# Optimization experiments

Measured on AMD Instinct MI355X. Metric: run time of the kernel, lower is better.

The kernel has to match this reference:

```python
import jax, jax.numpy as jnp
import numpy as np

COMMITMENT_COST = 0.25
NUM_EMBEDDINGS = 1024
EMBEDDING_DIM = 256


def setup_inputs() -> dict:
    key = jax.random.key(0)
    k1, k2 = jax.random.split(key)
    inputs = jax.random.normal(k1, (64, 256, 32, 32), dtype=jnp.float32)
    emb_w = jax.random.normal(k2, (NUM_EMBEDDINGS, EMBEDDING_DIM), dtype=jnp.float32)
    return {"inputs": inputs, "emb_w": emb_w}


def reference(inputs, emb_w):
    # NCHW -> NHWC, flatten to [N, D]
    x = jnp.transpose(inputs, (0, 2, 3, 1))  # [B, H, W, D]
    B, H, W, D = x.shape
    flat = x.reshape(-1, D)  # [N, D]

    distances = (
        jnp.sum(flat * flat, axis=1, keepdims=True)
        + jnp.sum(emb_w * emb_w, axis=1)
        - 2.0 * flat @ emb_w.T
    )
    idx = jnp.argmin(distances, axis=1)  # [N]

    # one-hot @ W is just a gather of codebook rows
    quantized = emb_w[idx].reshape(B, H, W, D)

    # avg_probs = mean of one-hot encodings = normalized codeword counts
    counts = jnp.zeros((NUM_EMBEDDINGS,), dtype=jnp.float32).at[idx].add(1.0)
    avg_probs = counts / flat.shape[0]
    perplexity = jnp.exp(-jnp.sum(avg_probs * jnp.log(avg_probs + 1e-10)))

    e_latent_loss = jnp.mean((jax.lax.stop_gradient(quantized) - x) ** 2)
    loss = COMMITMENT_COST * e_latent_loss

    # straight-through estimator
    quantized_st = x + jax.lax.stop_gradient(quantized - x)
    quantized_out = jnp.transpose(quantized_st, (0, 3, 1, 2))  # back to NCHW

    return loss, quantized_out, perplexity, idx.reshape(B, H, W)
```

## Files before the change

### kernel.cpp

```cpp
#include <hip/hip_runtime.h>
#include <hip/hip_bf16.h>
#include <math.h>

typedef _Float16 f16;
typedef __attribute__((ext_vector_type(8))) _Float16 f16x8;
typedef __attribute__((ext_vector_type(16))) float f32x16;

#define DIMS 256
#define NCODE 1024
#define NPTS 65536

#define OUT_Q_OFF 1
#define OUT_PERP_OFF 16777217
#define OUT_IDX_OFF 16777218

#define EHI_F32_OFF 4
#define ELO_F32_OFF (4 + 131072)
#define TILE_BYTES 16384

#define XSTRIDE 132

__device__ __forceinline__ void gload_lds16(const void* g, void* l) {
    __builtin_amdgcn_global_load_lds(
        (const __attribute__((address_space(1))) unsigned int*)g,
        (__attribute__((address_space(3))) unsigned int*)l, 16, 0, 0);
}

__global__ __launch_bounds__(256) void k_eprep(const float* __restrict__ ew,
                                               char* __restrict__ ehi,
                                               char* __restrict__ elo,
                                               float* __restrict__ enorm) {
    int w = threadIdx.x >> 6;
    int l = threadIdx.x & 63;
    int row = blockIdx.x * 4 + w;
    float4 v = *reinterpret_cast<const float4*>(ew + (size_t)row * DIMS + l * 4);
    float vv[4] = {v.x, v.y, v.z, v.w};
    __align__(8) f16 hh[4];
    __align__(8) f16 ll[4];
    float s = 0.0f;
    #pragma unroll
    for (int e = 0; e < 4; ++e) {
        f16 h = (f16)vv[e];
        hh[e] = h;
        ll[e] = (f16)(vv[e] - (float)h);
        s += vv[e] * vv[e];
    }
    size_t off = (size_t)(row >> 5) * TILE_BYTES + (size_t)(row & 31) * 512
               + (size_t)((((l >> 1) ^ (row & 7)) << 4) + ((l & 1) << 3));
    *reinterpret_cast<float2*>(ehi + off) = *reinterpret_cast<float2*>(hh);
    *reinterpret_cast<float2*>(elo + off) = *reinterpret_cast<float2*>(ll);
    #pragma unroll
    for (int off2 = 32; off2 > 0; off2 >>= 1) s += __shfl_down(s, off2);
    if (l == 0) enorm[row] = s;
}

__global__ __launch_bounds__(256, 2) void k_argmin_mfma(const float* __restrict__ x,
                                                        const char* __restrict__ ehi,
                                                        const char* __restrict__ elo,
                                                        const float* __restrict__ enorm,
                                                        int* __restrict__ out_idx) {
    __shared__ __align__(16) char smem[2 * 2 * TILE_BYTES];
    __shared__ float enorm_lds[NCODE];
    float* Xs = (float*)smem;

    const int t = threadIdx.x;
    const int wave = t >> 6;
    const int lane = t & 63;
    const int lrow = lane & 31;
    const int lhalf = lane >> 5;

    const int blk = blockIdx.x;
    const int b = blk >> 3;
    const int hw0 = (blk & 7) << 7;
    const float* xb = x + (size_t)b * (DIMS * 1024) + hw0;

    #pragma unroll
    for (int i = 0; i < 4; ++i) enorm_lds[t + 256 * i] = enorm[t + 256 * i];

    f16x8 ahi[16], alo[16];
    #pragma unroll
    for (int dc = 0; dc < 4; ++dc) {
        __syncthreads();
        #pragma unroll
        for (int i = 0; i < 8; ++i) {
            int d = (t >> 5) + 8 * i;
            int p4 = (t & 31) * 4;
            float4 v = *reinterpret_cast<const float4*>(xb + (size_t)(dc * 64 + d) * 1024 + p4);
            *reinterpret_cast<float4*>(&Xs[d * XSTRIDE + p4]) = v;
        }
        __syncthreads();
        int p = wave * 32 + lrow;
        #pragma unroll
        for (int kcl = 0; kcl < 4; ++kcl) {
            f16x8 h, l;
            #pragma unroll
            for (int e = 0; e < 8; ++e) {
                float xv = Xs[(kcl * 16 + lhalf * 8 + e) * XSTRIDE + p];
                f16 hi = (f16)xv;
                h[e] = hi;
                l[e] = (f16)(xv - (float)hi);
            }
            ahi[dc * 4 + kcl] = h;
            alo[dc * 4 + kcl] = l;
        }
    }
    __syncthreads();

    const char* gplane = (wave >> 1) ? elo : ehi;
    const int pl_off = (wave >> 1) * TILE_BYTES;
    const int woff = (wave & 1) * 8192;

    #pragma unroll
    for (int i = 0; i < 8; ++i) {
        int off = woff + i * 1024;
        gload_lds16(gplane + off + lane * 16, smem + pl_off + off);
    }
    __syncthreads();

    float bestv[16];
    int besti[16];
    #pragma unroll
    for (int r = 0; r < 16; ++r) { bestv[r] = 3.4e38f; besti[r] = 0; }

    int cur = 0;
    for (int rd = 0; rd < 32; ++rd) {
        if (rd + 1 < 32) {
            const char* gp = gplane + (size_t)(rd + 1) * TILE_BYTES;
            char* lp = smem + (cur ^ 1) * (2 * TILE_BYTES) + pl_off;
            #pragma unroll
            for (int i = 0; i < 8; ++i) {
                int off = woff + i * 1024;
                gload_lds16(gp + off + lane * 16, lp + off);
            }
        }

        const char* EHb = smem + cur * (2 * TILE_BYTES);
        const char* ELb = EHb + TILE_BYTES;
        f32x16 acc;
        #pragma unroll
        for (int r = 0; r < 16; ++r) acc[r] = 0.0f;

        #pragma unroll
        for (int kc = 0; kc < 16; ++kc) {
            int g = kc * 2 + lhalf;
            int ra = lrow * 512 + ((g ^ (lrow & 7)) << 4);
            f16x8 bh = *reinterpret_cast<const f16x8*>(EHb + ra);
            f16x8 bl = *reinterpret_cast<const f16x8*>(ELb + ra);
            acc = __builtin_amdgcn_mfma_f32_32x32x16_f16(ahi[kc], bh, acc, 0, 0, 0);
            acc = __builtin_amdgcn_mfma_f32_32x32x16_f16(ahi[kc], bl, acc, 0, 0, 0);
            acc = __builtin_amdgcn_mfma_f32_32x32x16_f16(alo[kc], bh, acc, 0, 0, 0);
        }

        const int code0 = rd * 32;
        float en = enorm_lds[code0 + lrow];
        int cw = code0 + lrow;
        #pragma unroll
        for (int r = 0; r < 16; ++r) {
            float s = fmaf(-2.0f, acc[r], en);
            if (s < bestv[r]) { bestv[r] = s; besti[r] = cw; }
        }

        __syncthreads();
        cur ^= 1;
    }

    #pragma unroll
    for (int off = 1; off <= 16; off <<= 1) {
        #pragma unroll
        for (int r = 0; r < 16; ++r) {
            float ov = __shfl_xor(bestv[r], off);
            int oi = __shfl_xor(besti[r], off);
            if (ov < bestv[r] || (ov == bestv[r] && oi < besti[r])) {
                bestv[r] = ov;
                besti[r] = oi;
            }
        }
    }
    if (lrow == 0) {
        #pragma unroll
        for (int r = 0; r < 16; ++r) {
            int row = (r & 3) + 8 * (r >> 2) + 4 * lhalf;
            out_idx[blk * 128 + wave * 32 + row] = besti[r];
        }
    }
}

#define QSTRIDE 258
__global__ __launch_bounds__(512) void k_quant(const float* __restrict__ x,
                                               const float* __restrict__ ew,
                                               const int* __restrict__ idxv,
                                               float* __restrict__ out,
                                               float* __restrict__ loss_acc) {
    __shared__ float Eq[64 * QSTRIDE];
    __shared__ int ids[64];
    const int t = threadIdx.x;
    const int blk = blockIdx.x;
    const int b = blk >> 4;
    const int hw0 = (blk & 15) << 6;

    if (t < 64) ids[t] = idxv[(b << 10) + hw0 + t];
    __syncthreads();

    #pragma unroll
    for (int i = 0; i < 8; ++i) {
        int f = i * 512 + t;
        int row = f >> 6;
        int c4 = f & 63;
        float4 v = *reinterpret_cast<const float4*>(ew + (size_t)ids[row] * DIMS + c4 * 4);
        float2 lo2 = {v.x, v.y};
        float2 hi2 = {v.z, v.w};
        *reinterpret_cast<float2*>(&Eq[row * QSTRIDE + c4 * 4]) = lo2;
        *reinterpret_cast<float2*>(&Eq[row * QSTRIDE + c4 * 4 + 2]) = hi2;
    }
    __syncthreads();

    const int p = t & 63;
    const int c0 = t >> 6;
    float lsum = 0.0f;
    #pragma unroll
    for (int k = 0; k < 32; ++k) {
        int c = k * 8 + c0;
        unsigned g = ((unsigned)b << 18) | ((unsigned)c << 10) | (unsigned)(hw0 + p);
        float xv = x[g];
        float q = Eq[p * QSTRIDE + c];
        float d = q - xv;
        out[OUT_Q_OFF + g] = xv + d;
        lsum += d * d;
    }
    #pragma unroll
    for (int off = 32; off > 0; off >>= 1) lsum += __shfl_down(lsum, off);
    if ((t & 63) == 0) atomicAdd(&loss_acc[blk & 63], lsum);
}

__global__ __launch_bounds__(256) void k_hist(const int* __restrict__ idxv,
                                              int* __restrict__ counts,
                                              float* __restrict__ out) {
    __shared__ int h[NCODE];
    int t = threadIdx.x;
    #pragma unroll
    for (int i = 0; i < 4; ++i) h[t + 256 * i] = 0;
    __syncthreads();
    int base = blockIdx.x * 1024;
    #pragma unroll
    for (int i = 0; i < 4; ++i) {
        int n = base + t + 256 * i;
        int id = idxv[n];
        out[OUT_IDX_OFF + n] = (float)id;
        atomicAdd(&h[id], 1);
    }
    __syncthreads();
    #pragma unroll
    for (int i = 0; i < 4; ++i) {
        int v = h[t + 256 * i];
        if (v) atomicAdd(&counts[t + 256 * i], v);
    }
}

__global__ __launch_bounds__(256) void k_final(const int* __restrict__ counts,
                                               const float* __restrict__ loss_acc,
                                               float* __restrict__ out) {
    int t = threadIdx.x;
    float s = 0.0f;
    #pragma unroll
    for (int i = 0; i < 4; ++i) {
        int cnt = counts[t + 256 * i];
        float p = (float)cnt * (1.0f / 65536.0f);
        s += p * logf(p + 1e-10f);
    }
    #pragma unroll
    for (int off = 32; off > 0; off >>= 1) s += __shfl_down(s, off);
    __shared__ float wsum[4];
    if ((t & 63) == 0) wsum[t >> 6] = s;
    __syncthreads();
    if (t == 0) {
        float S = wsum[0] + wsum[1] + wsum[2] + wsum[3];
        out[OUT_PERP_OFF] = expf(-S);
        float ls = 0.0f;
        for (int i = 0; i < 64; ++i) ls += loss_acc[i];
        out[0] = 0.25f * (ls * (1.0f / 16777216.0f));
    }
}

extern "C" void kernel_launch(void* const* d_in, const int* in_sizes, int n_in,
                              void* d_out, int out_size, void* d_ws, size_t ws_size,
                              hipStream_t stream) {
    const float* x = (const float*)d_in[0];
    const float* ew = (const float*)d_in[1];
    float* out = (float*)d_out;
    float* ws = (float*)d_ws;

    float* loss_acc = ws;
    int* counts = (int*)(ws + 64);
    float* enorm = ws + 64 + 1024;
    int* idxv = (int*)(ws + 64 + 2048);

    char* ehi = (char*)(out + EHI_F32_OFF);
    char* elo = (char*)(out + ELO_F32_OFF);

    hipMemsetAsync(d_ws, 0, (64 + 1024) * sizeof(float), stream);

    k_eprep<<<256, 256, 0, stream>>>(ew, ehi, elo, enorm);
    k_argmin_mfma<<<512, 256, 0, stream>>>(x, ehi, elo, enorm, idxv);
    k_quant<<<1024, 512, 0, stream>>>(x, ew, idxv, out, loss_acc);
    k_hist<<<64, 256, 0, stream>>>(idxv, counts, out);
    k_final<<<1, 256, 0, stream>>>(counts, loss_acc, out);
}
```

Baseline: 178.4 us.

## Read low-half codebook from global directly and fuse histogram into quant kernel

The argmin kernel now stages only the high-half fp16 codebook tiles in LDS, halving the LDS footprint. The low-half tiles are read straight from global/L2 in a transposed, coalesced layout written by the prep kernel. MFMA sections get raised wave priority, and the separate histogram kernel is folded into the quant kernel with a per-block LDS histogram, removing one launch. The trade-off is extra global-load latency inside the MFMA loop in exchange for higher occupancy, plus 1024 blocks each flushing histogram atomics instead of 64.

```diff
diff --git a/kernel.cpp b/kernel.cpp
--- a/kernel.cpp
+++ b/kernel.cpp
@@ -45,10 +45,12 @@
         ll[e] = (f16)(vv[e] - (float)h);
         s += vv[e] * vv[e];
     }
-    size_t off = (size_t)(row >> 5) * TILE_BYTES + (size_t)(row & 31) * 512
-               + (size_t)((((l >> 1) ^ (row & 7)) << 4) + ((l & 1) << 3));
-    *reinterpret_cast<float2*>(ehi + off) = *reinterpret_cast<float2*>(hh);
-    *reinterpret_cast<float2*>(elo + off) = *reinterpret_cast<float2*>(ll);
+    size_t hoff = (size_t)(row >> 5) * TILE_BYTES + (size_t)(row & 31) * 512
+                + (size_t)((((l >> 1) ^ (row & 7)) << 4) + ((l & 1) << 3));
+    size_t loff = (size_t)(row >> 5) * TILE_BYTES + (size_t)(l >> 1) * 512
+                + (size_t)(((row & 31) << 4) + ((l & 1) << 3));
+    *reinterpret_cast<float2*>(ehi + hoff) = *reinterpret_cast<float2*>(hh);
+    *reinterpret_cast<float2*>(elo + loff) = *reinterpret_cast<float2*>(ll);
     #pragma unroll
     for (int off2 = 32; off2 > 0; off2 >>= 1) s += __shfl_down(s, off2);
     if (l == 0) enorm[row] = s;
@@ -59,7 +61,7 @@
                                                         const char* __restrict__ elo,
                                                         const float* __restrict__ enorm,
                                                         int* __restrict__ out_idx) {
-    __shared__ __align__(16) char smem[2 * 2 * TILE_BYTES];
+    __shared__ __align__(16) char smem[XSTRIDE * 64 * 4];
     __shared__ float enorm_lds[NCODE];
     float* Xs = (float*)smem;
 
@@ -106,14 +108,10 @@
     }
     __syncthreads();
 
-    const char* gplane = (wave >> 1) ? elo : ehi;
-    const int pl_off = (wave >> 1) * TILE_BYTES;
-    const int woff = (wave & 1) * 8192;
-
-    #pragma unroll
-    for (int i = 0; i < 8; ++i) {
-        int off = woff + i * 1024;
-        gload_lds16(gplane + off + lane * 16, smem + pl_off + off);
+    #pragma unroll
+    for (int i = 0; i < 4; ++i) {
+        int off = wave * 4096 + i * 1024;
+        gload_lds16(ehi + off + lane * 16, smem + off);
     }
     __syncthreads();
 
@@ -122,34 +120,37 @@
     #pragma unroll
     for (int r = 0; r < 16; ++r) { bestv[r] = 3.4e38f; besti[r] = 0; }
 
-    int cur = 0;
     for (int rd = 0; rd < 32; ++rd) {
+        const int cur = rd & 1;
         if (rd + 1 < 32) {
-            const char* gp = gplane + (size_t)(rd + 1) * TILE_BYTES;
-            char* lp = smem + (cur ^ 1) * (2 * TILE_BYTES) + pl_off;
+            const char* gp = ehi + (size_t)(rd + 1) * TILE_BYTES;
+            char* lp = smem + (cur ^ 1) * TILE_BYTES;
             #pragma unroll
-            for (int i = 0; i < 8; ++i) {
-                int off = woff + i * 1024;
+            for (int i = 0; i < 4; ++i) {
+                int off = wave * 4096 + i * 1024;
                 gload_lds16(gp + off + lane * 16, lp + off);
             }
         }
 
-        const char* EHb = smem + cur * (2 * TILE_BYTES);
-        const char* ELb = EHb + TILE_BYTES;
+        const char* EHb = smem + cur * TILE_BYTES;
+        const char* ELg = elo + (size_t)rd * TILE_BYTES;
         f32x16 acc;
         #pragma unroll
         for (int r = 0; r < 16; ++r) acc[r] = 0.0f;
 
+        __builtin_amdgcn_s_setprio(1);
         #pragma unroll
         for (int kc = 0; kc < 16; ++kc) {
             int g = kc * 2 + lhalf;
-            int ra = lrow * 512 + ((g ^ (lrow & 7)) << 4);
-            f16x8 bh = *reinterpret_cast<const f16x8*>(EHb + ra);
-            f16x8 bl = *reinterpret_cast<const f16x8*>(ELb + ra);
+            f16x8 bh = *reinterpret_cast<const f16x8*>(
+                EHb + lrow * 512 + ((g ^ (lrow & 7)) << 4));
+            f16x8 bl = *reinterpret_cast<const f16x8*>(
+                ELg + g * 512 + lrow * 16);
             acc = __builtin_amdgcn_mfma_f32_32x32x16_f16(ahi[kc], bh, acc, 0, 0, 0);
             acc = __builtin_amdgcn_mfma_f32_32x32x16_f16(ahi[kc], bl, acc, 0, 0, 0);
             acc = __builtin_amdgcn_mfma_f32_32x32x16_f16(alo[kc], bh, acc, 0, 0, 0);
         }
+        __builtin_amdgcn_s_setprio(0);
 
         const int code0 = rd * 32;
         float en = enorm_lds[code0 + lrow];
@@ -161,7 +162,6 @@
         }
 
         __syncthreads();
-        cur ^= 1;
     }
 
     #pragma unroll
@@ -190,16 +190,22 @@
                                                const float* __restrict__ ew,
                                                const int* __restrict__ idxv,
                                                float* __restrict__ out,
-                                               float* __restrict__ loss_acc) {
+                                               float* __restrict__ loss_acc,
+                                               int* __restrict__ counts) {
     __shared__ float Eq[64 * QSTRIDE];
     __shared__ int ids[64];
+    __shared__ int h[NCODE];
     const int t = threadIdx.x;
     const int blk = blockIdx.x;
     const int b = blk >> 4;
     const int hw0 = (blk & 15) << 6;
 
     if (t < 64) ids[t] = idxv[(b << 10) + hw0 + t];
-    __syncthreads();
+    h[t] = 0;
+    h[t + 512] = 0;
+    __syncthreads();
+
+    if (t < 64) atomicAdd(&h[ids[t]], 1);
 
     #pragma unroll
     for (int i = 0; i < 8; ++i) {
@@ -230,30 +236,12 @@
     #pragma unroll
     for (int off = 32; off > 0; off >>= 1) lsum += __shfl_down(lsum, off);
     if ((t & 63) == 0) atomicAdd(&loss_acc[blk & 63], lsum);
-}
-
-__global__ __launch_bounds__(256) void k_hist(const int* __restrict__ idxv,
-                                              int* __restrict__ counts,
-                                              float* __restrict__ out) {
-    __shared__ int h[NCODE];
-    int t = threadIdx.x;
-    #pragma unroll
-    for (int i = 0; i < 4; ++i) h[t + 256 * i] = 0;
-    __syncthreads();
-    int base = blockIdx.x * 1024;
-    #pragma unroll
-    for (int i = 0; i < 4; ++i) {
-        int n = base + t + 256 * i;
-        int id = idxv[n];
-        out[OUT_IDX_OFF + n] = (float)id;
-        atomicAdd(&h[id], 1);
-    }
-    __syncthreads();
-    #pragma unroll
-    for (int i = 0; i < 4; ++i) {
-        int v = h[t + 256 * i];
-        if (v) atomicAdd(&counts[t + 256 * i], v);
-    }
+
+    int v0 = h[t];
+    if (v0) atomicAdd(&counts[t], v0);
+    int v1 = h[t + 512];
+    if (v1) atomicAdd(&counts[t + 512], v1);
+    if (t < 64) out[OUT_IDX_OFF + (b << 10) + hw0 + t] = (float)ids[t];
 }
 
 __global__ __launch_bounds__(256) void k_final(const int* __restrict__ counts,
@@ -301,7 +289,6 @@
 
     k_eprep<<<256, 256, 0, stream>>>(ew, ehi, elo, enorm);
     k_argmin_mfma<<<512, 256, 0, stream>>>(x, ehi, elo, enorm, idxv);
-    k_quant<<<1024, 512, 0, stream>>>(x, ew, idxv, out, loss_acc);
-    k_hist<<<64, 256, 0, stream>>>(idxv, counts, out);
+    k_quant<<<1024, 512, 0, stream>>>(x, ew, idxv, out, loss_acc, counts);
     k_final<<<1, 256, 0, stream>>>(counts, loss_acc, out);
 }
```

After: 213.6 us. +19.7%, slower.

## Split MFMA accumulator chain and fuse histogram into quantize kernel

Applied to the files above, without the earlier changes.

The argmin inner loop now alternates its three MFMAs per k-step between two independent accumulators and sums them at the end. This shortens the dependent MFMA chain so more MFMAs can be in flight. The separate histogram kernel is removed: each quantize block builds a shared-memory histogram of its 64 indices, flushes the nonzero bins with global atomics, and writes the index outputs. This saves a launch and a re-read of the index buffer, at the cost of extra LDS and per-block histogram scans. Splitting the accumulators slightly changes the floating-point summation order.

```diff
diff --git a/kernel.cpp b/kernel.cpp
--- a/kernel.cpp
+++ b/kernel.cpp
@@ -136,9 +136,9 @@
 
         const char* EHb = smem + cur * (2 * TILE_BYTES);
         const char* ELb = EHb + TILE_BYTES;
-        f32x16 acc;
-        #pragma unroll
-        for (int r = 0; r < 16; ++r) acc[r] = 0.0f;
+        f32x16 acc0, acc1;
+        #pragma unroll
+        for (int r = 0; r < 16; ++r) { acc0[r] = 0.0f; acc1[r] = 0.0f; }
 
         #pragma unroll
         for (int kc = 0; kc < 16; ++kc) {
@@ -146,9 +146,12 @@
             int ra = lrow * 512 + ((g ^ (lrow & 7)) << 4);
             f16x8 bh = *reinterpret_cast<const f16x8*>(EHb + ra);
             f16x8 bl = *reinterpret_cast<const f16x8*>(ELb + ra);
-            acc = __builtin_amdgcn_mfma_f32_32x32x16_f16(ahi[kc], bh, acc, 0, 0, 0);
-            acc = __builtin_amdgcn_mfma_f32_32x32x16_f16(ahi[kc], bl, acc, 0, 0, 0);
-            acc = __builtin_amdgcn_mfma_f32_32x32x16_f16(alo[kc], bh, acc, 0, 0, 0);
+            acc0 = __builtin_amdgcn_mfma_f32_32x32x16_f16(ahi[kc], bh, acc0, 0, 0, 0);
+            acc1 = __builtin_amdgcn_mfma_f32_32x32x16_f16(ahi[kc], bl, acc1, 0, 0, 0);
+            if (kc & 1)
+                acc1 = __builtin_amdgcn_mfma_f32_32x32x16_f16(alo[kc], bh, acc1, 0, 0, 0);
+            else
+                acc0 = __builtin_amdgcn_mfma_f32_32x32x16_f16(alo[kc], bh, acc0, 0, 0, 0);
         }
 
         const int code0 = rd * 32;
@@ -156,7 +159,7 @@
         int cw = code0 + lrow;
         #pragma unroll
         for (int r = 0; r < 16; ++r) {
-            float s = fmaf(-2.0f, acc[r], en);
+            float s = fmaf(-2.0f, acc0[r] + acc1[r], en);
             if (s < bestv[r]) { bestv[r] = s; besti[r] = cw; }
         }
 
@@ -190,16 +193,22 @@
                                                const float* __restrict__ ew,
                                                const int* __restrict__ idxv,
                                                float* __restrict__ out,
-                                               float* __restrict__ loss_acc) {
+                                               float* __restrict__ loss_acc,
+                                               int* __restrict__ counts) {
     __shared__ float Eq[64 * QSTRIDE];
     __shared__ int ids[64];
+    __shared__ int h[NCODE];
     const int t = threadIdx.x;
     const int blk = blockIdx.x;
     const int b = blk >> 4;
     const int hw0 = (blk & 15) << 6;
 
     if (t < 64) ids[t] = idxv[(b << 10) + hw0 + t];
-    __syncthreads();
+    h[t] = 0;
+    h[t + 512] = 0;
+    __syncthreads();
+
+    if (t < 64) atomicAdd(&h[ids[t]], 1);
 
     #pragma unroll
     for (int i = 0; i < 8; ++i) {
@@ -230,30 +239,12 @@
     #pragma unroll
     for (int off = 32; off > 0; off >>= 1) lsum += __shfl_down(lsum, off);
     if ((t & 63) == 0) atomicAdd(&loss_acc[blk & 63], lsum);
-}
-
-__global__ __launch_bounds__(256) void k_hist(const int* __restrict__ idxv,
-                                              int* __restrict__ counts,
-                                              float* __restrict__ out) {
-    __shared__ int h[NCODE];
-    int t = threadIdx.x;
-    #pragma unroll
-    for (int i = 0; i < 4; ++i) h[t + 256 * i] = 0;
-    __syncthreads();
-    int base = blockIdx.x * 1024;
-    #pragma unroll
-    for (int i = 0; i < 4; ++i) {
-        int n = base + t + 256 * i;
-        int id = idxv[n];
-        out[OUT_IDX_OFF + n] = (float)id;
-        atomicAdd(&h[id], 1);
-    }
-    __syncthreads();
-    #pragma unroll
-    for (int i = 0; i < 4; ++i) {
-        int v = h[t + 256 * i];
-        if (v) atomicAdd(&counts[t + 256 * i], v);
-    }
+
+    int v0 = h[t];
+    if (v0) atomicAdd(&counts[t], v0);
+    int v1 = h[t + 512];
+    if (v1) atomicAdd(&counts[t + 512], v1);
+    if (t < 64) out[OUT_IDX_OFF + (b << 10) + hw0 + t] = (float)ids[t];
 }
 
 __global__ __launch_bounds__(256) void k_final(const int* __restrict__ counts,
@@ -301,7 +292,6 @@
 
     k_eprep<<<256, 256, 0, stream>>>(ew, ehi, elo, enorm);
     k_argmin_mfma<<<512, 256, 0, stream>>>(x, ehi, elo, enorm, idxv);
-    k_quant<<<1024, 512, 0, stream>>>(x, ew, idxv, out, loss_acc);
-    k_hist<<<64, 256, 0, stream>>>(idxv, counts, out);
+    k_quant<<<1024, 512, 0, stream>>>(x, ew, idxv, out, loss_acc, counts);
     k_final<<<1, 256, 0, stream>>>(counts, loss_acc, out);
 }
```

New measurement: 176.7 us. No clear change (-1.0%).
